# Kernel optimization log

Measured on AMD Instinct MI355X. Metric: run time of the kernel, lower is better.

Reference implementation:

```python
import jax, jax.numpy as jnp
import numpy as np

L, S, N, E = 2048, 2048, 4, 1024
FF = 4 * E


def _ln(x, g, b, eps=1e-5):
    m = jnp.mean(x, axis=-1, keepdims=True)
    v = jnp.mean((x - m) ** 2, axis=-1, keepdims=True)
    return (x - m) * jax.lax.rsqrt(v + eps) * g + b


def _attn(q_in, k_in, v_in, qw, kw, vw, in_b, ow, ob, mask):
    # q_in: [L,N,E], k_in/v_in: [S,N,E]; single head, head_dim == E
    e = q_in.shape[-1]
    scale = float(e) ** -0.5
    q = (q_in @ qw.T + in_b[:e]) * scale          # [L,N,E]
    k = k_in @ kw.T + in_b[e:2 * e]               # [S,N,E]
    v = v_in @ vw.T + in_b[2 * e:]                # [S,N,E]
    scores = jnp.einsum('lne,sne->nls', q, k)     # [N,L,S]
    if mask is not None:
        scores = scores + mask[None]
    w = jax.nn.softmax(scores, axis=-1)
    out = jnp.einsum('nls,sne->lne', w, v)        # [L,N,E]
    return out @ ow.T + ob


def setup_inputs() -> dict:
    key = jax.random.key(0)
    ks = jax.random.split(key, 24)
    g = lambda k, shape: jax.random.normal(k, shape, dtype=jnp.float32) * 0.02
    causal = jnp.where(jnp.triu(jnp.ones((L, L), dtype=bool), 1), -1e9, 0.0).astype(jnp.float32)
    return {
        'tgt': jax.random.normal(ks[0], (L, N, E), dtype=jnp.float32),
        'memory': jax.random.normal(ks[1], (S, N, E), dtype=jnp.float32),
        'tgt_mask': causal,
        'sa_qw': g(ks[2], (E, E)), 'sa_kw': g(ks[3], (E, E)), 'sa_vw': g(ks[4], (E, E)),
        'sa_b': jnp.zeros((3 * E,), jnp.float32),
        'sa_ow': g(ks[5], (E, E)), 'sa_ob': jnp.zeros((E,), jnp.float32),
        'ca_qw': g(ks[6], (E, E)), 'ca_kw': g(ks[7], (E, E)), 'ca_vw': g(ks[8], (E, E)),
        'ca_b': jnp.zeros((3 * E,), jnp.float32),
        'ca_ow': g(ks[9], (E, E)), 'ca_ob': jnp.zeros((E,), jnp.float32),
        'ln1_g': jnp.ones((E,), jnp.float32), 'ln1_b': jnp.zeros((E,), jnp.float32),
        'ln2_g': jnp.ones((E,), jnp.float32), 'ln2_b': jnp.zeros((E,), jnp.float32),
        'ln3_g': jnp.ones((E,), jnp.float32), 'ln3_b': jnp.zeros((E,), jnp.float32),
        'w1': g(ks[10], (FF, E)), 'b1': jnp.zeros((FF,), jnp.float32),
        'w2': g(ks[11], (E, FF)), 'b2': jnp.zeros((E,), jnp.float32),
    }


def reference(tgt, memory, tgt_mask,
              sa_qw, sa_kw, sa_vw, sa_b, sa_ow, sa_ob,
              ca_qw, ca_kw, ca_vw, ca_b, ca_ow, ca_ob,
              ln1_g, ln1_b, ln2_g, ln2_b, ln3_g, ln3_b,
              w1, b1, w2, b2):
    x = tgt
    # pre-norm self-attention with causal mask (dropout_p=0, eval)
    h = _ln(x, ln1_g, ln1_b)
    x = x + _attn(h, h, h, sa_qw, sa_kw, sa_vw, sa_b, sa_ow, sa_ob, tgt_mask)
    # pre-norm cross-attention over encoder memory
    h = _ln(x, ln2_g, ln2_b)
    x = x + _attn(h, memory, memory, ca_qw, ca_kw, ca_vw, ca_b, ca_ow, ca_ob, None)
    h = _ln(x, ln3_g, ln3_b)
    h = h @ w1.T + b1
    h = h * jax.nn.sigmoid(1.702 * h)
    x = x + (h @ w2.T + b2)
    return x
```

## Files before the change

### kernel.cpp

```cpp
#include <hip/hip_runtime.h>
#include <hip/hip_bf16.h>
#include <cstdint>
#include <cstddef>


using bf16_t = __bf16;
typedef __bf16 bf16x8 __attribute__((ext_vector_type(8)));
typedef __bf16 bf16x4 __attribute__((ext_vector_type(4)));
typedef float f32x4 __attribute__((ext_vector_type(4)));

__device__ __forceinline__ void gll16(const void* g, void* lds) {
  __builtin_amdgcn_global_load_lds(
      (__attribute__((address_space(1))) void*)(g),
      (__attribute__((address_space(3))) void*)(lds), 16, 0, 0);
}

__global__ __launch_bounds__(256) void f32_to_bf16_n(
    const float* __restrict__ in, bf16_t* __restrict__ out, int n) {
  const size_t i = ((size_t)blockIdx.x * 256 + threadIdx.x) * 8;
  if (i >= (size_t)n) return;
  f32x4 a = *(const f32x4*)(in + i);
  f32x4 b = *(const f32x4*)(in + i + 4);
  bf16x8 v;
#pragma unroll
  for (int j = 0; j < 4; ++j) { v[j] = (bf16_t)a[j]; v[4 + j] = (bf16_t)b[j]; }
  *(bf16x8*)(out + i) = v;
}

struct CastSeg { const float* src; bf16_t* dst; int chunks; };
struct CastDesc { CastSeg s[16]; };
__global__ __launch_bounds__(256) void cast_multi(CastDesc d) {
  int blk = blockIdx.x, seg = 0, base = 0;
  while (blk - base >= d.s[seg].chunks) { base += d.s[seg].chunks; ++seg; }
  const size_t i = (size_t)(blk - base) * 1024 + threadIdx.x * 4;
  f32x4 a = *(const f32x4*)(d.s[seg].src + i);
  bf16x4 v;
#pragma unroll
  for (int j = 0; j < 4; ++j) v[j] = (bf16_t)a[j];
  *(bf16x4*)(d.s[seg].dst + i) = v;
}

__global__ __launch_bounds__(256) void ln_kernel(
    const float* __restrict__ x, const float* __restrict__ g,
    const float* __restrict__ b, bf16_t* __restrict__ out) {
  const int row = blockIdx.x, tid = threadIdx.x;
  const float* xr = x + (size_t)row * 1024;
  float v0 = xr[tid], v1 = xr[tid + 256], v2 = xr[tid + 512], v3 = xr[tid + 768];
  float s = v0 + v1 + v2 + v3;
  float ss = v0 * v0 + v1 * v1 + v2 * v2 + v3 * v3;
#pragma unroll
  for (int off = 32; off > 0; off >>= 1) {
    s += __shfl_down(s, off, 64);
    ss += __shfl_down(ss, off, 64);
  }
  __shared__ float red[8];
  const int w = tid >> 6, lane = tid & 63;
  if (lane == 0) { red[w] = s; red[4 + w] = ss; }
  __syncthreads();
  s = red[0] + red[1] + red[2] + red[3];
  ss = red[4] + red[5] + red[6] + red[7];
  const float mean = s * (1.f / 1024.f);
  float var = ss * (1.f / 1024.f) - mean * mean;
  var = var < 0.f ? 0.f : var;
  const float inv = rsqrtf(var + 1e-5f);
  bf16_t* orow = out + (size_t)row * 1024;
  orow[tid]       = (bf16_t)((v0 - mean) * inv * g[tid]       + b[tid]);
  orow[tid + 256] = (bf16_t)((v1 - mean) * inv * g[tid + 256] + b[tid + 256]);
  orow[tid + 512] = (bf16_t)((v2 - mean) * inv * g[tid + 512] + b[tid + 512]);
  orow[tid + 768] = (bf16_t)((v3 - mean) * inv * g[tid + 768] + b[tid + 768]);
}

template <int CAUSAL>
__global__ __launch_bounds__(256) void softmax_kernel(bf16_t* __restrict__ sc) {
  const int row = blockIdx.x, tid = threadIdx.x;
  const int l = row & 2047;
  bf16_t* sr = sc + (size_t)row * 2048;
  float v[8];
  float mx = -3.4e38f;
#pragma unroll
  for (int i = 0; i < 8; ++i) {
    const int j = tid + i * 256;
    v[i] = (CAUSAL && j > l) ? -3.4e38f : (float)sr[j];
    mx = fmaxf(mx, v[i]);
  }
#pragma unroll
  for (int off = 32; off > 0; off >>= 1) mx = fmaxf(mx, __shfl_down(mx, off, 64));
  __shared__ float red[8];
  const int w = tid >> 6, lane = tid & 63;
  if (lane == 0) red[w] = mx;
  __syncthreads();
  mx = fmaxf(fmaxf(red[0], red[1]), fmaxf(red[2], red[3]));
  float sum = 0.f;
#pragma unroll
  for (int i = 0; i < 8; ++i) { v[i] = __expf(v[i] - mx); sum += v[i]; }
#pragma unroll
  for (int off = 32; off > 0; off >>= 1) sum += __shfl_down(sum, off, 64);
  if (lane == 0) red[4 + w] = sum;
  __syncthreads();
  sum = red[4] + red[5] + red[6] + red[7];
  const float r = 1.f / sum;
#pragma unroll
  for (int i = 0; i < 8; ++i) sr[tid + i * 256] = (bf16_t)(v[i] * r);
}

__global__ __launch_bounds__(256) void transpose_v(const bf16_t* __restrict__ v,
                                                   bf16_t* __restrict__ vt) {
  __shared__ bf16_t tile[64][72];
  const int n = blockIdx.z;
  const int s0 = blockIdx.x * 64, e0 = blockIdx.y * 64;
  const int tid = threadIdx.x;
#pragma unroll
  for (int j = 0; j < 2; ++j) {
    int flat = j * 256 + tid;
    int r = flat >> 3, c8 = (flat & 7) * 8;
    bf16x8 val = *(const bf16x8*)(v + ((size_t)(s0 + r) * 4 + n) * 1024 + e0 + c8);
#pragma unroll
    for (int i = 0; i < 8; ++i) tile[r][c8 + i] = val[i];
  }
  __syncthreads();
#pragma unroll
  for (int j = 0; j < 2; ++j) {
    int flat = j * 256 + tid;
    int er = flat >> 3, s8 = (flat & 7) * 8;
    bf16x8 val;
#pragma unroll
    for (int i = 0; i < 8; ++i) val[i] = tile[s8 + i][er];
    *(bf16x8*)(vt + ((size_t)n * 1024 + e0 + er) * 2048 + s0 + s8) = val;
  }
}

template <int EPI, int MODE, int NS>
__global__ __launch_bounds__(256) void gemm_bt(
    const bf16_t* __restrict__ A, const bf16_t* __restrict__ Aalt,
    long lda, long sA,
    const bf16_t* __restrict__ W0, const bf16_t* __restrict__ W1,
    const bf16_t* __restrict__ W2, long ldw, long sW,
    void* __restrict__ C0, void* __restrict__ C1, void* __restrict__ C2,
    long ldc, long sC,
    const bf16_t* __restrict__ bias, const float* __restrict__ res,
    float scale, int K) {
  const size_t row0 = (size_t)blockIdx.y * 128;
  const size_t col0 = (size_t)blockIdx.x * 128;
  if (MODE == 1 && col0 > row0) return;
  const int z = blockIdx.z;
  constexpr int BK = NS * 32;

  const bf16_t* Ap = (MODE == 3) ? (z == 0 ? A : Aalt) : A + (size_t)z * sA;
  const bf16_t* Wp = (MODE == 3) ? (z == 0 ? W0 : (z == 1 ? W1 : W2))
                                 : W0 + (size_t)z * sW;
  void* Cp = (MODE == 3) ? (z == 0 ? C0 : (z == 1 ? C1 : C2)) : C0;
  const size_t zoffC = (MODE == 3) ? 0 : (size_t)z * sC;
  const bf16_t* biasp = bias ? bias + (MODE == 3 ? z * 1024 : 0) : nullptr;
  const float scl = (MODE == 3 && z != 0) ? 1.f : scale;
  const int kend = (MODE == 2) ? min(K, (int)row0 + 128) : K;

  __shared__ __align__(16) bf16_t As[2][NS][128 * 32];
  __shared__ __align__(16) bf16_t Bs[2][NS][128 * 32];
  const int tid = threadIdx.x;
  const int wv = tid >> 6, lane = tid & 63;
  const int quad = lane >> 4, l15 = lane & 15;
  const int wr = wv >> 1, wc = wv & 1;

  const bf16_t* gA[2 * NS];
  const bf16_t* gW[2 * NS];
  int lbase[2 * NS];
#pragma unroll
  for (int j = 0; j < 2 * NS; ++j) {
    const int c = wv * (128 * NS) + j * 64 + lane;
    const int ks = c >> 9;
    const int rr = (c & 511) >> 2;
    const int cc = ks * 32 + (c & 3) * 8;
    gA[j] = Ap + (row0 + rr) * lda + cc;
    gW[j] = Wp + (col0 + rr) * ldw + cc;
    lbase[j] = (wv * (128 * NS) + j * 64) * 8;
  }

  f32x4 acc[4][4];
#pragma unroll
  for (int mi = 0; mi < 4; ++mi)
#pragma unroll
    for (int ni = 0; ni < 4; ++ni) acc[mi][ni] = (f32x4)0.f;

#pragma unroll
  for (int j = 0; j < 2 * NS; ++j) {
    gll16(gA[j], &As[0][0][0] + lbase[j]);
    gll16(gW[j], &Bs[0][0][0] + lbase[j]);
  }

  int p = 0;
  for (int k0 = 0; k0 < kend; k0 += BK, p ^= 1) {
    __syncthreads();
    const int kn = k0 + BK;
    if (kn < kend) {
#pragma unroll
      for (int j = 0; j < 2 * NS; ++j) {
        gll16(gA[j] + kn, &As[p ^ 1][0][0] + lbase[j]);
        gll16(gW[j] + kn, &Bs[p ^ 1][0][0] + lbase[j]);
      }
    }
#pragma unroll
    for (int ks = 0; ks < NS; ++ks) {
      bf16x8 af[4], bfv[4];
#pragma unroll
      for (int mi = 0; mi < 4; ++mi)
        af[mi] = *(const bf16x8*)(As[p][ks] + (wr * 64 + mi * 16 + l15) * 32 + quad * 8);
#pragma unroll
      for (int ni = 0; ni < 4; ++ni)
        bfv[ni] = *(const bf16x8*)(Bs[p][ks] + (wc * 64 + ni * 16 + l15) * 32 + quad * 8);
#pragma unroll
      for (int mi = 0; mi < 4; ++mi)
#pragma unroll
        for (int ni = 0; ni < 4; ++ni)
          acc[mi][ni] = __builtin_amdgcn_mfma_f32_16x16x32_bf16(
              af[mi], bfv[ni], acc[mi][ni], 0, 0, 0);
    }
  }

  float* Cf = (float*)Cp;
  bf16_t* Cb = (bf16_t*)Cp;
#pragma unroll
  for (int mi = 0; mi < 4; ++mi) {
    const size_t gr = row0 + wr * 64 + mi * 16 + quad * 4;
#pragma unroll
    for (int ni = 0; ni < 4; ++ni) {
      const size_t gc = col0 + wc * 64 + ni * 16 + l15;
      float bv = 0.f;
      if (EPI == 0 || EPI == 2 || EPI == 3) bv = biasp ? (float)biasp[gc] : 0.f;
#pragma unroll
      for (int r = 0; r < 4; ++r) {
        float v = acc[mi][ni][r];
        const size_t idx = zoffC + (gr + r) * ldc + gc;
        if (EPI == 0) {
          Cb[idx] = (bf16_t)((v + bv) * scl);
        } else if (EPI == 1) {
          Cb[idx] = (bf16_t)v;
        } else if (EPI == 2) {
          Cf[idx] = res[idx] + v + bv;
        } else {
          float t = v + bv;
          Cb[idx] = (bf16_t)(t * (1.f / (1.f + __expf(-1.702f * t))));
        }
      }
    }
  }
}

template <int EPI, int MODE, int NS = 1>
static void launch_gemm(hipStream_t stream, int M, int N, int Z,
                        const void* A, const void* Aalt, long lda, long sA,
                        const void* W0, const void* W1, const void* W2,
                        long ldw, long sW,
                        void* C0, void* C1, void* C2, long ldc, long sC,
                        const void* bias, const float* res, float scale, int K) {
  dim3 grid(N / 128, M / 128, Z);
  gemm_bt<EPI, MODE, NS><<<grid, dim3(256), 0, stream>>>(
      (const bf16_t*)A, (const bf16_t*)Aalt, lda, sA,
      (const bf16_t*)W0, (const bf16_t*)W1, (const bf16_t*)W2, ldw, sW,
      C0, C1, C2, ldc, sC, (const bf16_t*)bias, res, scale, K);
}

extern "C" void kernel_launch(void* const* d_in, const int* in_sizes, int n_in,
                              void* d_out, int out_size, void* d_ws, size_t ws_size,
                              hipStream_t stream) {
  (void)in_sizes; (void)n_in; (void)out_size; (void)ws_size;
  const float* tgt  = (const float*)d_in[0];
  const float* mem  = (const float*)d_in[1];
  const float* sa_qw = (const float*)d_in[3];
  const float* sa_kw = (const float*)d_in[4];
  const float* sa_vw = (const float*)d_in[5];
  const float* sa_b  = (const float*)d_in[6];
  const float* sa_ow = (const float*)d_in[7];
  const float* sa_ob = (const float*)d_in[8];
  const float* ca_qw = (const float*)d_in[9];
  const float* ca_kw = (const float*)d_in[10];
  const float* ca_vw = (const float*)d_in[11];
  const float* ca_b  = (const float*)d_in[12];
  const float* ca_ow = (const float*)d_in[13];
  const float* ca_ob = (const float*)d_in[14];
  const float* ln1g = (const float*)d_in[15];
  const float* ln1b = (const float*)d_in[16];
  const float* ln2g = (const float*)d_in[17];
  const float* ln2b = (const float*)d_in[18];
  const float* ln3g = (const float*)d_in[19];
  const float* ln3b = (const float*)d_in[20];
  const float* w1 = (const float*)d_in[21];
  const float* b1 = (const float*)d_in[22];
  const float* w2 = (const float*)d_in[23];
  const float* b2 = (const float*)d_in[24];

  char* ws = (char*)d_ws;
  const size_t MB = 1048576;
  float*  xf   = (float*)(ws);
  bf16_t* hb   = (bf16_t*)(ws + 32 * MB);
  bf16_t* vb   = (bf16_t*)(ws + 48 * MB);
  bf16_t* qb   = (bf16_t*)(ws + 64 * MB);
  bf16_t* kb   = (bf16_t*)(ws + 80 * MB);
  bf16_t* vt   = (bf16_t*)(ws + 96 * MB);
  bf16_t* sb   = (bf16_t*)(ws + 32 * MB);
  bf16_t* ao   = kb;
  bf16_t* hid  = (bf16_t*)(ws + 48 * MB);
  bf16_t* memb = (bf16_t*)(ws + 112 * MB);
  bf16_t* wt   = (bf16_t*)(ws + 128 * MB);
  bf16_t* bb   = (bf16_t*)(ws + 160 * MB);

  const size_t M1 = 1048576;
  bf16_t* saq = wt,          *sak = wt + M1,     *sav = wt + 2 * M1;
  bf16_t* sao = wt + 3 * M1, *caq = wt + 4 * M1, *cak = wt + 5 * M1;
  bf16_t* cav = wt + 6 * M1, *cao = wt + 7 * M1;
  bf16_t* w1b = wt + 8 * M1;
  bf16_t* w2b = wt + 12 * M1;

  const float qscale = 0.03125f;

  CastDesc cd;
  auto seg = [&](int i, const float* s, bf16_t* d, int elems) {
    cd.s[i] = CastSeg{s, d, elems / 1024};
  };
  seg(0, sa_qw, saq, 1 << 20);  seg(1, sa_kw, sak, 1 << 20);
  seg(2, sa_vw, sav, 1 << 20);  seg(3, sa_ow, sao, 1 << 20);
  seg(4, ca_qw, caq, 1 << 20);  seg(5, ca_kw, cak, 1 << 20);
  seg(6, ca_vw, cav, 1 << 20);  seg(7, ca_ow, cao, 1 << 20);
  seg(8, w1, w1b, 1 << 22);     seg(9, w2, w2b, 1 << 22);
  seg(10, sa_b, bb, 3072);      seg(11, sa_ob, bb + 3072, 1024);
  seg(12, ca_b, bb + 4096, 3072); seg(13, ca_ob, bb + 7168, 1024);
  seg(14, b1, bb + 8192, 4096); seg(15, b2, bb + 12288, 1024);
  int total_chunks = 0;
  for (int i = 0; i < 16; ++i) total_chunks += cd.s[i].chunks;
  cast_multi<<<total_chunks, 256, 0, stream>>>(cd);
  f32_to_bf16_n<<<4096, 256, 0, stream>>>(mem, memb, 1 << 23);

  ln_kernel<<<8192, 256, 0, stream>>>(tgt, ln1g, ln1b, hb);
  launch_gemm<0, 3>(stream, 8192, 1024, 3, hb, hb, 1024, 0,
                    saq, sak, sav, 1024, 0, qb, kb, vb, 1024, 0,
                    bb, nullptr, qscale, 1024);
  transpose_v<<<dim3(32, 16, 4), 256, 0, stream>>>(vb, vt);
  launch_gemm<1, 1>(stream, 2048, 2048, 4, qb, nullptr, 4096, 1024,
                    kb, nullptr, nullptr, 4096, 1024,
                    sb, nullptr, nullptr, 2048, 4194304, nullptr, nullptr,
                    1.f, 1024);
  softmax_kernel<1><<<8192, 256, 0, stream>>>(sb);
  launch_gemm<0, 2, 2>(stream, 2048, 1024, 4, sb, nullptr, 2048, 4194304,
                       vt, nullptr, nullptr, 2048, 2097152,
                       ao, nullptr, nullptr, 4096, 1024, nullptr, nullptr,
                       1.f, 2048);
  launch_gemm<2, 0, 2>(stream, 8192, 1024, 1, ao, nullptr, 1024, 0,
                       sao, nullptr, nullptr, 1024, 0,
                       xf, nullptr, nullptr, 1024, 0, bb + 3072, tgt,
                       1.f, 1024);

  ln_kernel<<<8192, 256, 0, stream>>>(xf, ln2g, ln2b, hb);
  launch_gemm<0, 3>(stream, 8192, 1024, 3, hb, memb, 1024, 0,
                    caq, cak, cav, 1024, 0, qb, kb, vb, 1024, 0,
                    bb + 4096, nullptr, qscale, 1024);
  transpose_v<<<dim3(32, 16, 4), 256, 0, stream>>>(vb, vt);
  launch_gemm<1, 0>(stream, 2048, 2048, 4, qb, nullptr, 4096, 1024,
                    kb, nullptr, nullptr, 4096, 1024,
                    sb, nullptr, nullptr, 2048, 4194304, nullptr, nullptr,
                    1.f, 1024);
  softmax_kernel<0><<<8192, 256, 0, stream>>>(sb);
  launch_gemm<0, 0, 2>(stream, 2048, 1024, 4, sb, nullptr, 2048, 4194304,
                       vt, nullptr, nullptr, 2048, 2097152,
                       ao, nullptr, nullptr, 4096, 1024, nullptr, nullptr,
                       1.f, 2048);
  launch_gemm<2, 0, 2>(stream, 8192, 1024, 1, ao, nullptr, 1024, 0,
                       cao, nullptr, nullptr, 1024, 0,
                       xf, nullptr, nullptr, 1024, 0, bb + 7168, xf,
                       1.f, 1024);

  ln_kernel<<<8192, 256, 0, stream>>>(xf, ln3g, ln3b, hb);
  launch_gemm<3, 0>(stream, 8192, 4096, 1, hb, nullptr, 1024, 0,
                    w1b, nullptr, nullptr, 1024, 0,
                    hid, nullptr, nullptr, 4096, 0, bb + 8192, nullptr,
                    1.f, 1024);
  launch_gemm<2, 0, 2>(stream, 8192, 1024, 1, hid, nullptr, 4096, 0,
                       w2b, nullptr, nullptr, 4096, 0,
                       d_out, nullptr, nullptr, 1024, 0, bb + 12288, xf,
                       1.f, 4096);
}
```

Measured before the change: 858.7 us.

## Add 256x256 tiled bf16 GEMM kernel with deep async pipeline for QKV, scores, FFN1

Introduces a new 512-thread GEMM kernel using 256x256 output tiles, a 4-phase per-K-step pipeline with global_load_lds prefetch six stages ahead, and XCD-aware workgroup remapping. It replaces the 128x128 GEMM for the QKV projections, the QK^T score GEMMs and the first FFN GEMM. Larger tiles raise arithmetic intensity and cut LDS/global traffic per FLOP, while setprio and explicit waitcnt and barriers are meant to overlap loads with MFMA. The tradeoffs are fewer workgroups (wave quantization on the causal score GEMM, which skips upper tiles), 64KB of LDS and high register pressure.

```diff
diff --git a/kernel.cpp b/kernel.cpp
--- a/kernel.cpp
+++ b/kernel.cpp
@@ -245,6 +245,152 @@
   }
 }
 
+template <int EPI, int MODE>
+__global__ __launch_bounds__(512, 2) void gemm256(
+    const bf16_t* __restrict__ A, const bf16_t* __restrict__ Aalt,
+    long lda, long sA,
+    const bf16_t* __restrict__ W0, const bf16_t* __restrict__ W1,
+    const bf16_t* __restrict__ W2, long ldw, long sW,
+    void* __restrict__ C0, void* __restrict__ C1, void* __restrict__ C2,
+    long ldc, long sC,
+    const bf16_t* __restrict__ bias, float scale, int K) {
+  const int gx = gridDim.x, gy = gridDim.y;
+  const int nwg = gx * gy * (int)gridDim.z;
+  const int hw = (int)blockIdx.x + gx * ((int)blockIdx.y + gy * (int)blockIdx.z);
+  const int logical = (hw & 7) * (nwg >> 3) + (hw >> 3);
+  const int bx = logical % gx;
+  const int by = (logical / gx) % gy;
+  const int z  = logical / (gx * gy);
+  const size_t row0 = (size_t)by * 256, col0 = (size_t)bx * 256;
+  if (MODE == 1 && bx > by) return;
+
+  const bf16_t* Ap = (MODE == 3) ? (z == 0 ? A : Aalt) : A + (size_t)z * sA;
+  const bf16_t* Wp = (MODE == 3) ? (z == 0 ? W0 : (z == 1 ? W1 : W2))
+                                 : W0 + (size_t)z * sW;
+  void* Cp = (MODE == 3) ? (z == 0 ? C0 : (z == 1 ? C1 : C2)) : C0;
+  const size_t zoffC = (MODE == 3) ? 0 : (size_t)z * sC;
+  const bf16_t* biasp = bias ? bias + (MODE == 3 ? z * 1024 : 0) : nullptr;
+  const float scl = (MODE == 3 && z != 0) ? 1.f : scale;
+
+  __shared__ __align__(16) bf16_t As[2][2][8192];
+  __shared__ __align__(16) bf16_t Bs[2][2][8192];
+
+  const int tid = threadIdx.x;
+  const int lane = tid & 63, wid = tid >> 6;
+  const int l15 = lane & 15, quad = lane >> 4;
+  const int wm = wid >> 2, wn = wid & 3;
+
+  const int srow = wid * 16 + (lane >> 2);
+  const int scol = (lane & 3) * 8;
+  const bf16_t* sAg0 = Ap + (row0 + srow) * lda + scol;
+  const bf16_t* sAg1 = Ap + (row0 + 128 + srow) * lda + scol;
+  const bf16_t* sBg0 = Wp + (col0 + srow) * ldw + scol;
+  const bf16_t* sBg1 = Wp + (col0 + 128 + srow) * ldw + scol;
+  const int ldso0 = (wid * 64) * 8;
+  const int ldso1 = (512 + wid * 64) * 8;
+
+  const int T = K >> 6;
+  const int HT = 4 * T;
+
+  auto stage = [&](int h) {
+    if (h >= HT) return;
+    const int u = h >> 2, ks = (h >> 1) & 1;
+    const int coff = u * 64 + ks * 32;
+    if (h & 1) {
+      gll16(sBg0 + coff, &Bs[u & 1][ks][0] + ldso0);
+      gll16(sBg1 + coff, &Bs[u & 1][ks][0] + ldso1);
+    } else {
+      gll16(sAg0 + coff, &As[u & 1][ks][0] + ldso0);
+      gll16(sAg1 + coff, &As[u & 1][ks][0] + ldso1);
+    }
+  };
+
+  f32x4 acc[2][4][4];
+#pragma unroll
+  for (int mh = 0; mh < 2; ++mh)
+#pragma unroll
+    for (int mi = 0; mi < 4; ++mi)
+#pragma unroll
+      for (int ni = 0; ni < 4; ++ni) acc[mh][mi][ni] = (f32x4)0.f;
+
+#pragma unroll
+  for (int h = 0; h < 6; ++h) stage(h);
+
+  const int aoff = (wm * 128 + l15) * 32 + quad * 8;
+  const int boff = (wn * 64 + l15) * 32 + quad * 8;
+
+  for (int t = 0; t < T; ++t) {
+    const int p = t & 1;
+    const int g4 = 4 * t;
+    bf16x8 bfv[4];
+
+#define PHASE(PH, KK, MH)                                                     \
+    {                                                                         \
+      stage(g4 + 6 + PH);                                                     \
+      bf16x8 af[4];                                                           \
+      if (PH == 0) {                                                          \
+                 \
+        if (t + 1 < T) asm volatile("s_waitcnt vmcnt(6)" ::: "memory");       \
+        else           asm volatile("s_waitcnt vmcnt(0)" ::: "memory");       \
+        __builtin_amdgcn_s_barrier();                                         \
+      }                                                                       \
+      _Pragma("unroll")                                                       \
+      for (int mi = 0; mi < 4; ++mi)                                          \
+        af[mi] = *(const bf16x8*)(&As[p][KK][0] + aoff + (MH * 64 + mi * 16) * 32); \
+      if (MH == 0) {                                                          \
+        _Pragma("unroll")                                                     \
+        for (int ni = 0; ni < 4; ++ni)                                        \
+          bfv[ni] = *(const bf16x8*)(&Bs[p][KK][0] + boff + (ni * 16) * 32);  \
+      }                                                                       \
+      if (PH != 0) __builtin_amdgcn_s_barrier();                              \
+      asm volatile("s_waitcnt lgkmcnt(0)" ::: "memory");                      \
+      __builtin_amdgcn_sched_barrier(0);                                      \
+      __builtin_amdgcn_s_setprio(1);                                          \
+      _Pragma("unroll")                                                       \
+      for (int mi = 0; mi < 4; ++mi)                                          \
+        _Pragma("unroll")                                                     \
+        for (int ni = 0; ni < 4; ++ni)                                        \
+          acc[MH][mi][ni] = __builtin_amdgcn_mfma_f32_16x16x32_bf16(          \
+              af[mi], bfv[ni], acc[MH][mi][ni], 0, 0, 0);                     \
+      __builtin_amdgcn_s_setprio(0);                                          \
+      __builtin_amdgcn_s_barrier();                                           \
+    }
+
+    PHASE(0, 0, 0)
+    PHASE(1, 0, 1)
+    PHASE(2, 1, 0)
+    PHASE(3, 1, 1)
+#undef PHASE
+  }
+
+  bf16_t* Cb = (bf16_t*)Cp;
+#pragma unroll
+  for (int mh = 0; mh < 2; ++mh)
+#pragma unroll
+    for (int mi = 0; mi < 4; ++mi) {
+      const size_t gr = row0 + wm * 128 + mh * 64 + mi * 16 + quad * 4;
+#pragma unroll
+      for (int ni = 0; ni < 4; ++ni) {
+        const size_t gc = col0 + wn * 64 + ni * 16 + l15;
+        float bv = 0.f;
+        if (EPI == 0 || EPI == 3) bv = biasp ? (float)biasp[gc] : 0.f;
+#pragma unroll
+        for (int r = 0; r < 4; ++r) {
+          const float v = acc[mh][mi][ni][r];
+          const size_t idx = zoffC + (gr + r) * ldc + gc;
+          if (EPI == 0) {
+            Cb[idx] = (bf16_t)((v + bv) * scl);
+          } else if (EPI == 1) {
+            Cb[idx] = (bf16_t)v;
+          } else {
+            const float tt = v + bv;
+            Cb[idx] = (bf16_t)(tt * (1.f / (1.f + __expf(-1.702f * tt))));
+          }
+        }
+      }
+    }
+}
+
 template <int EPI, int MODE, int NS = 1>
 static void launch_gemm(hipStream_t stream, int M, int N, int Z,
                         const void* A, const void* Aalt, long lda, long sA,
@@ -257,6 +403,20 @@
       (const bf16_t*)A, (const bf16_t*)Aalt, lda, sA,
       (const bf16_t*)W0, (const bf16_t*)W1, (const bf16_t*)W2, ldw, sW,
       C0, C1, C2, ldc, sC, (const bf16_t*)bias, res, scale, K);
+}
+
+template <int EPI, int MODE>
+static void launch_gemm256(hipStream_t stream, int M, int N, int Z,
+                           const void* A, const void* Aalt, long lda, long sA,
+                           const void* W0, const void* W1, const void* W2,
+                           long ldw, long sW,
+                           void* C0, void* C1, void* C2, long ldc, long sC,
+                           const void* bias, float scale, int K) {
+  dim3 grid(N / 256, M / 256, Z);
+  gemm256<EPI, MODE><<<grid, dim3(512), 0, stream>>>(
+      (const bf16_t*)A, (const bf16_t*)Aalt, lda, sA,
+      (const bf16_t*)W0, (const bf16_t*)W1, (const bf16_t*)W2, ldw, sW,
+      C0, C1, C2, ldc, sC, (const bf16_t*)bias, scale, K);
 }
 
 extern "C" void kernel_launch(void* const* d_in, const int* in_sizes, int n_in,
@@ -330,14 +490,14 @@
   f32_to_bf16_n<<<4096, 256, 0, stream>>>(mem, memb, 1 << 23);
 
   ln_kernel<<<8192, 256, 0, stream>>>(tgt, ln1g, ln1b, hb);
-  launch_gemm<0, 3>(stream, 8192, 1024, 3, hb, hb, 1024, 0,
-                    saq, sak, sav, 1024, 0, qb, kb, vb, 1024, 0,
-                    bb, nullptr, qscale, 1024);
+  launch_gemm256<0, 3>(stream, 8192, 1024, 3, hb, hb, 1024, 0,
+                       saq, sak, sav, 1024, 0, qb, kb, vb, 1024, 0,
+                       bb, qscale, 1024);
   transpose_v<<<dim3(32, 16, 4), 256, 0, stream>>>(vb, vt);
-  launch_gemm<1, 1>(stream, 2048, 2048, 4, qb, nullptr, 4096, 1024,
-                    kb, nullptr, nullptr, 4096, 1024,
-                    sb, nullptr, nullptr, 2048, 4194304, nullptr, nullptr,
-                    1.f, 1024);
+  launch_gemm256<1, 1>(stream, 2048, 2048, 4, qb, nullptr, 4096, 1024,
+                       kb, nullptr, nullptr, 4096, 1024,
+                       sb, nullptr, nullptr, 2048, 4194304, nullptr,
+                       1.f, 1024);
   softmax_kernel<1><<<8192, 256, 0, stream>>>(sb);
   launch_gemm<0, 2, 2>(stream, 2048, 1024, 4, sb, nullptr, 2048, 4194304,
                        vt, nullptr, nullptr, 2048, 2097152,
@@ -349,14 +509,14 @@
                        1.f, 1024);
 
   ln_kernel<<<8192, 256, 0, stream>>>(xf, ln2g, ln2b, hb);
-  launch_gemm<0, 3>(stream, 8192, 1024, 3, hb, memb, 1024, 0,
-                    caq, cak, cav, 1024, 0, qb, kb, vb, 1024, 0,
-                    bb + 4096, nullptr, qscale, 1024);
+  launch_gemm256<0, 3>(stream, 8192, 1024, 3, hb, memb, 1024, 0,
+                       caq, cak, cav, 1024, 0, qb, kb, vb, 1024, 0,
+                       bb + 4096, qscale, 1024);
   transpose_v<<<dim3(32, 16, 4), 256, 0, stream>>>(vb, vt);
-  launch_gemm<1, 0>(stream, 2048, 2048, 4, qb, nullptr, 4096, 1024,
-                    kb, nullptr, nullptr, 4096, 1024,
-                    sb, nullptr, nullptr, 2048, 4194304, nullptr, nullptr,
-                    1.f, 1024);
+  launch_gemm256<1, 0>(stream, 2048, 2048, 4, qb, nullptr, 4096, 1024,
+                       kb, nullptr, nullptr, 4096, 1024,
+                       sb, nullptr, nullptr, 2048, 4194304, nullptr,
+                       1.f, 1024);
   softmax_kernel<0><<<8192, 256, 0, stream>>>(sb);
   launch_gemm<0, 0, 2>(stream, 2048, 1024, 4, sb, nullptr, 2048, 4194304,
                        vt, nullptr, nullptr, 2048, 2097152,
@@ -368,10 +528,10 @@
                        1.f, 1024);
 
   ln_kernel<<<8192, 256, 0, stream>>>(xf, ln3g, ln3b, hb);
-  launch_gemm<3, 0>(stream, 8192, 4096, 1, hb, nullptr, 1024, 0,
-                    w1b, nullptr, nullptr, 1024, 0,
-                    hid, nullptr, nullptr, 4096, 0, bb + 8192, nullptr,
-                    1.f, 1024);
+  launch_gemm256<3, 0>(stream, 8192, 4096, 1, hb, nullptr, 1024, 0,
+                       w1b, nullptr, nullptr, 1024, 0,
+                       hid, nullptr, nullptr, 4096, 0, bb + 8192,
+                       1.f, 1024);
   launch_gemm<2, 0, 2>(stream, 8192, 1024, 1, hid, nullptr, 4096, 0,
                        w2b, nullptr, nullptr, 4096, 0,
                        d_out, nullptr, nullptr, 1024, 0, bb + 12288, xf,
```

After: 838.9 us. 2.3% less time.
